# Kernel optimization log

Hardware: AMD Instinct MI355X
Metric: run time of the kernel (lower is better)

## Reference

```python
import jax, jax.numpy as jnp
import numpy as np

# SparseSphereConv (graph_level=6 -> V=40962, kernel_size=9, stride=1, select_index=None)
# Pipeline: neighbor gather -> data-dependent nonzero row selection ->
# per-vertex KxK interpolation matmul -> 1xK conv (linear over C_in,K) -> scatter back.
# With stride=1 / select_index=None the static selection is the identity, so the
# dynamic nonzero selection is equivalent to computing all rows and zeroing the
# rows whose gathered features are entirely zero (selected rows are scattered back,
# unselected rows stay 0 in sparse_reset's zero-initialized output).

BS, C_IN, C_OUT, V, K = 4, 32, 32, 40962, 9

def setup_inputs() -> dict:
    key = jax.random.key(0)
    k1, k2, k3, k4, k5 = jax.random.split(key, 5)
    x = jax.random.normal(k1, (BS, C_IN, V), dtype=jnp.float32)
    index = jax.random.randint(k2, (V, K), 0, V, dtype=jnp.int32)          # neighbor ids per vertex
    itp_mat = jax.random.uniform(k3, (V, K, K), dtype=jnp.float32)         # per-vertex interpolation
    conv_w = jax.random.normal(k4, (C_OUT, C_IN, K), dtype=jnp.float32) * 0.05  # Conv2d(C_in,C_out,(1,K)) weight
    conv_b = jax.random.normal(k5, (C_OUT,), dtype=jnp.float32) * 0.05
    return {"x": x, "index": index, "itp_mat": itp_mat, "conv_w": conv_w, "conv_b": conv_b}

def reference(x, index, itp_mat, conv_w, conv_b):
    # x: [bs, C, V] -> permute(2,0,1) -> gather neighbors -> [V, K, bs, C]
    g = jnp.transpose(x, (2, 0, 1))[index]
    g = jnp.transpose(g, (3, 2, 0, 1))                      # [C, bs, V, K]  (== reshape of [C, bs*V, K])
    # sparse_prepare: keep rows whose min or max over (C, K) is nonzero (detached in torch)
    gd = jax.lax.stop_gradient(g)
    rmin = gd.min(axis=(0, 3))                              # [bs, V]
    rmax = gd.max(axis=(0, 3))                              # [bs, V]
    mask = (rmin != 0) | (rmax != 0)                        # [bs, V]
    # Interploate: [C, S, 1, K] @ [S, K, K] per row -> batched small matmul
    interp = jnp.einsum('cbvk,vkj->cbvj', g, itp_mat)       # [C, bs, V, K]
    # Conv2d with kernel (1, K): contraction over (C_in, K) + bias
    out = jnp.einsum('cbvk,ock->bov', interp, conv_w) + conv_b[None, :, None]  # [bs, C_out, V]
    # sparse_reset: rows not selected stay zero
    return out * mask[:, None, :].astype(out.dtype)
```

## Files before the change

### kernel.cpp

```cpp
#include <hip/hip_runtime.h>
#include <hip/hip_bf16.h>

#define NV 40962
#define NK 9
#define CIN 32
#define COUT 32
#define NBS 4
#define VT 256
#define TP 260
#define NT 2561
#define PGRID 512
#define NV81 (NV * 81)
#define NV9  (NV * 9)

typedef __attribute__((ext_vector_type(8))) short bf16x8;
typedef __attribute__((ext_vector_type(4))) float f32x4;
typedef __attribute__((ext_vector_type(2))) float f32x2;

#define PKFMA_L(A, G, R) asm("v_pk_fma_f32 %0, %1, %2, %0 op_sel:[0,0,0] op_sel_hi:[0,1,1]" : "+v"(A) : "v"(G), "v"(R))
#define PKFMA_H(A, G, R) asm("v_pk_fma_f32 %0, %1, %2, %0 op_sel:[1,0,0] op_sel_hi:[1,1,1]" : "+v"(A) : "v"(G), "v"(R))
#define PKMUL_L(A, G, R) asm("v_pk_mul_f32 %0, %1, %2 op_sel:[0,0] op_sel_hi:[0,1]" : "=v"(A) : "v"(G), "v"(R))
#define PKMUL_H(A, G, R) asm("v_pk_mul_f32 %0, %1, %2 op_sel:[1,0] op_sel_hi:[1,1]" : "=v"(A) : "v"(G), "v"(R))

#define ACC(cc, j) ((j) == 8 ? acc8[cc] : (((j) & 1) ? acc2[cc][(j) >> 1].y \
                                                     : acc2[cc][(j) >> 1].x))

__device__ __forceinline__ unsigned pkbf(float a, float b) {
    union { __hip_bfloat162 h2; unsigned u; } cv;
    cv.h2 = __float22bfloat162_rn(make_float2(a, b));
    return cv.u;
}

__device__ __forceinline__ void bar_lgkm() {
    asm volatile("s_waitcnt lgkmcnt(0)\n\ts_barrier" ::: "memory");
}

__global__ void __launch_bounds__(256) transpose_x_bf16(
    const float* __restrict__ x, unsigned* __restrict__ xtw)
{
    __shared__ unsigned T[16 * TP];
    const int b  = blockIdx.x & 3;
    const int v0 = (blockIdx.x >> 2) * VT;
    const int t  = threadIdx.x;
    const int w  = t >> 6;
    const int L  = t & 63;
    const bool full = (v0 + VT <= NV);

    #pragma unroll
    for (int i = 0; i < 4; ++i) {
        const int q = w + 4 * i;
        const float* rowA = x + (size_t)(b * 32 + 2 * q) * NV;
        const float* rowB = rowA + NV;
        #pragma unroll
        for (int h = 0; h < 2; ++h) {
            const int vl = 128 * h + 2 * L;
            float2 a, c;
            if (full) {
                a = *(const float2*)(rowA + v0 + vl);
                c = *(const float2*)(rowB + v0 + vl);
            } else {
                const int v = v0 + vl;
                a.x = (v     < NV) ? rowA[v]     : 0.0f;
                a.y = (v + 1 < NV) ? rowA[v + 1] : 0.0f;
                c.x = (v     < NV) ? rowB[v]     : 0.0f;
                c.y = (v + 1 < NV) ? rowB[v + 1] : 0.0f;
            }
            uint2 d;
            d.x = pkbf(a.x, c.x);
            d.y = pkbf(a.y, c.y);
            *(uint2*)&T[q * TP + vl] = d;
        }
    }
    __syncthreads();

    #pragma unroll
    for (int i = 0; i < 4; ++i) {
        const int vl = i * 64 + w * 16 + (L >> 2);
        const int u4 = L & 3;
        const int v  = v0 + vl;
        if (v < NV) {
            uint4 d;
            d.x = T[(4 * u4 + 0) * TP + vl];
            d.y = T[(4 * u4 + 1) * TP + vl];
            d.z = T[(4 * u4 + 2) * TP + vl];
            d.w = T[(4 * u4 + 3) * TP + vl];
            *(uint4*)&xtw[(size_t)v * 64 + b * 16 + 4 * u4] = d;
        }
    }
}

__device__ __forceinline__ void load_itp(float itpv[3],
                                         const float* __restrict__ itp,
                                         int tile, int t)
{
    const size_t base = (size_t)tile * 1296;
    #pragma unroll
    for (int i = 0; i < 3; ++i) {
        const int o = i * 512 + t;
        itpv[i] = (o < 1296 && base + o < (size_t)NV81) ? itp[base + o] : 0.0f;
    }
}

__device__ __forceinline__ void stage_itp(float* __restrict__ buf,
                                          const float itpv[3], int t)
{
    #pragma unroll
    for (int i = 0; i < 3; ++i) {
        const int o = i * 512 + t;
        if (o < 1296) {
            const int vl = o / 81;
            const int r  = o - vl * 81;
            const int kk = r / 9;
            const int jj = r - kk * 9;
            buf[vl * 108 + kk * 12 + jj] = itpv[i];
        }
    }
}

__device__ __forceinline__ int load_idx(const int* __restrict__ index,
                                        int tile, int t)
{
    int r = 0;
    if (t < 144) {
        const size_t base = (size_t)tile * 144 + t;
        r = (base < (size_t)NV9) ? index[base] : 0;
    }
    return r;
}

__global__ void __launch_bounds__(512) sparse_conv_mfma(
    const unsigned short* __restrict__ xt, const int* __restrict__ index,
    const float* __restrict__ itp, const float* __restrict__ w,
    const float* __restrict__ bias, float* __restrict__ out)
{
    __shared__ unsigned Alds8[72 * 64 * 2];
    __shared__ unsigned short Wlds[36 * 32 * 8];
    __shared__ float itp_s[16 * 108];
    __shared__ int   idx_s[2][144];
    __shared__ unsigned long long nzb[8];

    const int t    = threadIdx.x;
    const int col  = t & 63;
    const int q    = t >> 6;
    const int b    = col >> 4;
    const int vloc = col & 15;
    const unsigned short* gb = xt + b * 32 + q * 4;

    int tile = blockIdx.x;

    #pragma unroll
    for (int r = 0; r < 3; ++r) {
        const int j = t + r * 512;
        if (j < 1152) {
            const int o = j & 31;
            const int c = j >> 5;
            const float4 f0 = *(const float4*)(w + o * 288 + c * 8);
            const float4 f1 = *(const float4*)(w + o * 288 + c * 8 + 4);
            uint4 d;
            d.x = pkbf(f0.x, f0.y); d.y = pkbf(f0.z, f0.w);
            d.z = pkbf(f1.x, f1.y); d.w = pkbf(f1.z, f1.w);
            *(uint4*)&Wlds[(c * 32 + o) * 8] = d;
        }
    }
    {
        const int i0 = load_idx(index, tile, t);
        const int i1 = load_idx(index, min(tile + PGRID, NT - 1), t);
        if (t < 144) { idx_s[0][t] = i0; idx_s[1][t] = i1; }
    }
    float itpv[3];
    load_itp(itpv, itp, tile, t);
    stage_itp(itp_s, itpv, t);
    __syncthreads();

    uint2 gath[NK];
    #pragma unroll
    for (int k = 0; k < NK; ++k) {
        const int nbr = idx_s[0][vloc * 9 + k];
        gath[k] = *(const uint2*)(gb + (size_t)nbr * 128);
    }
    load_itp(itpv, itp, min(tile + PGRID, NT - 1), t);
    int idxn = load_idx(index, min(tile + 2 * PGRID, NT - 1), t);
    int cur = 0;

    for (; tile < NT; tile += PGRID) {
        unsigned nzbits = 0;
        f32x2 acc2[4][4];
        float acc8[4];
        const float* ib = &itp_s[vloc * 108];

        #pragma unroll
        for (int k = 0; k < 4; ++k) {
            const uint2 gk = gath[k];
            nzbits |= (gk.x | gk.y) & 0x7FFF7FFFu;
            f32x2 gp01, gp23;
            gp01.x = __uint_as_float(gk.x << 16);
            gp01.y = __uint_as_float(gk.x & 0xFFFF0000u);
            gp23.x = __uint_as_float(gk.y << 16);
            gp23.y = __uint_as_float(gk.y & 0xFFFF0000u);
            const float* ir = ib + k * 12;
            f32x2 rp[4];
            rp[0] = *(const f32x2*)ir;       rp[1] = *(const f32x2*)(ir + 2);
            rp[2] = *(const f32x2*)(ir + 4); rp[3] = *(const f32x2*)(ir + 6);
            const float r8 = ir[8];
            if (k == 0) {
                #pragma unroll
                for (int jp = 0; jp < 4; ++jp) {
                    PKMUL_L(acc2[0][jp], gp01, rp[jp]);
                    PKMUL_H(acc2[1][jp], gp01, rp[jp]);
                    PKMUL_L(acc2[2][jp], gp23, rp[jp]);
                    PKMUL_H(acc2[3][jp], gp23, rp[jp]);
                }
                acc8[0] = gp01.x * r8; acc8[1] = gp01.y * r8;
                acc8[2] = gp23.x * r8; acc8[3] = gp23.y * r8;
            } else {
                #pragma unroll
                for (int jp = 0; jp < 4; ++jp) {
                    PKFMA_L(acc2[0][jp], gp01, rp[jp]);
                    PKFMA_H(acc2[1][jp], gp01, rp[jp]);
                    PKFMA_L(acc2[2][jp], gp23, rp[jp]);
                    PKFMA_H(acc2[3][jp], gp23, rp[jp]);
                }
                acc8[0] += gp01.x * r8; acc8[1] += gp01.y * r8;
                acc8[2] += gp23.x * r8; acc8[3] += gp23.y * r8;
            }
        }
        #pragma unroll
        for (int k = 0; k < 4; ++k) {
            const int nbr = idx_s[cur ^ 1][vloc * 9 + k];
            gath[k] = *(const uint2*)(gb + (size_t)nbr * 128);
        }
        #pragma unroll
        for (int k = 4; k < 9; ++k) {
            const uint2 gk = gath[k];
            nzbits |= (gk.x | gk.y) & 0x7FFF7FFFu;
            f32x2 gp01, gp23;
            gp01.x = __uint_as_float(gk.x << 16);
            gp01.y = __uint_as_float(gk.x & 0xFFFF0000u);
            gp23.x = __uint_as_float(gk.y << 16);
            gp23.y = __uint_as_float(gk.y & 0xFFFF0000u);
            const float* ir = ib + k * 12;
            f32x2 rp[4];
            rp[0] = *(const f32x2*)ir;       rp[1] = *(const f32x2*)(ir + 2);
            rp[2] = *(const f32x2*)(ir + 4); rp[3] = *(const f32x2*)(ir + 6);
            const float r8 = ir[8];
            #pragma unroll
            for (int jp = 0; jp < 4; ++jp) {
                PKFMA_L(acc2[0][jp], gp01, rp[jp]);
                PKFMA_H(acc2[1][jp], gp01, rp[jp]);
                PKFMA_L(acc2[2][jp], gp23, rp[jp]);
                PKFMA_H(acc2[3][jp], gp23, rp[jp]);
            }
            acc8[0] += gp01.x * r8; acc8[1] += gp01.y * r8;
            acc8[2] += gp23.x * r8; acc8[3] += gp23.y * r8;
        }
        #pragma unroll
        for (int k = 4; k < 9; ++k) {
            const int nbr = idx_s[cur ^ 1][vloc * 9 + k];
            gath[k] = *(const uint2*)(gb + (size_t)nbr * 128);
        }

        #pragma unroll
        for (int i2 = 0; i2 < 9; ++i2) {
            const int k0 = 4 * i2;
            const int h  = 9 * q + i2;
            uint2 d;
            d.x = pkbf(ACC(k0 / 9, k0 % 9),
                       ACC((k0 + 1) / 9, (k0 + 1) % 9));
            d.y = pkbf(ACC((k0 + 2) / 9, (k0 + 2) % 9),
                       ACC((k0 + 3) / 9, (k0 + 3) % 9));
            *(uint2*)&Alds8[(h * 64 + col) * 2] = d;
        }
        const unsigned long long bal = __ballot(nzbits != 0);
        if (col == 0) nzb[q] = bal;

        bar_lgkm();

        {
            const int dq = b;
            const int bb = q >> 1;
            const int oh = q & 1;
            const int colw = bb * 16 + vloc;

            f32x4 a0 = {0.f, 0.f, 0.f, 0.f};
            #pragma unroll
            for (int ks = 0; ks < 9; ++ks) {
                const int h0 = ks * 8 + dq * 2;
                const uint2 l2 = *(const uint2*)&Alds8[(h0 * 64 + colw) * 2];
                const uint2 h2 = *(const uint2*)&Alds8[((h0 + 1) * 64 + colw) * 2];
                union { uint4 u; bf16x8 v; } f;
                f.u.x = l2.x; f.u.y = l2.y; f.u.z = h2.x; f.u.w = h2.y;
                const int ch = ks * 4 + dq;
                const bf16x8 wa = *(const bf16x8*)&Wlds[(ch * 32 + oh * 16 + vloc) * 8];
                a0 = __builtin_amdgcn_mfma_f32_16x16x32_bf16(wa, f.v, a0, 0, 0, 0);
            }

            const unsigned long long nz = nzb[0] | nzb[1] | nzb[2] | nzb[3] |
                                          nzb[4] | nzb[5] | nzb[6] | nzb[7];
            const float m = ((nz >> colw) & 1ull) ? 1.0f : 0.0f;
            const int vv = tile * 16 + vloc;
            if (vv < NV) {
                float* outb = out + (size_t)bb * (COUT * NV) + vv;
                #pragma unroll
                for (int r = 0; r < 4; ++r) {
                    const int o = oh * 16 + dq * 4 + r;
                    outb[(size_t)o * NV] = (a0[r] + bias[o]) * m;
                }
            }
        }
        stage_itp(itp_s, itpv, t);
        if (t < 144) idx_s[cur][t] = idxn;
        load_itp(itpv, itp, min(tile + 2 * PGRID, NT - 1), t);
        idxn = load_idx(index, min(tile + 3 * PGRID, NT - 1), t);

        bar_lgkm();
        cur ^= 1;
    }
}

extern "C" void kernel_launch(void* const* d_in, const int* in_sizes, int n_in,
                              void* d_out, int out_size, void* d_ws, size_t ws_size,
                              hipStream_t stream)
{
    const float* x     = (const float*)d_in[0];
    const int*   index = (const int*)  d_in[1];
    const float* itp   = (const float*)d_in[2];
    const float* w     = (const float*)d_in[3];
    const float* bias  = (const float*)d_in[4];
    float*       out   = (float*)d_out;

    unsigned short* xt = (unsigned short*)d_ws;

    const int vtiles = (NV + VT - 1) / VT;
    hipLaunchKernelGGL(transpose_x_bf16, dim3(vtiles * NBS), dim3(256), 0,
                       stream, x, (unsigned*)xt);
    hipLaunchKernelGGL(sparse_conv_mfma, dim3(PGRID), dim3(512), 0,
                       stream, xt, index, itp, w, bias, out);
}
```

Measured before the change: 129.9 us.

## Move weight bf16 conversion to pre-kernel, remap waves per batch, raise grid

```diff
diff --git a/kernel.cpp b/kernel.cpp
--- a/kernel.cpp
+++ b/kernel.cpp
@@ -9,7 +9,7 @@
 #define VT 256
 #define TP 260
 #define NT 2561
-#define PGRID 512
+#define PGRID 768
 #define NV81 (NV * 81)
 #define NV9  (NV * 9)
 
@@ -89,6 +89,16 @@
     }
 }
 
+__global__ void __launch_bounds__(256) convert_w_bf16(
+    const float* __restrict__ w, unsigned short* __restrict__ wbf)
+{
+    const int i = blockIdx.x * 256 + threadIdx.x;
+    if (i < COUT * CIN * NK) {
+        unsigned u = __float_as_uint(w[i]);
+        wbf[i] = (unsigned short)((u + 0x7FFFu + ((u >> 16) & 1u)) >> 16);
+    }
+}
+
 __device__ __forceinline__ void load_itp(float itpv[3],
                                          const float* __restrict__ itp,
                                          int tile, int t)
@@ -130,38 +140,25 @@
 
 __global__ void __launch_bounds__(512) sparse_conv_mfma(
     const unsigned short* __restrict__ xt, const int* __restrict__ index,
-    const float* __restrict__ itp, const float* __restrict__ w,
+    const float* __restrict__ itp, const unsigned short* __restrict__ wbf,
     const float* __restrict__ bias, float* __restrict__ out)
 {
     __shared__ unsigned Alds8[72 * 64 * 2];
-    __shared__ unsigned short Wlds[36 * 32 * 8];
     __shared__ float itp_s[16 * 108];
     __shared__ int   idx_s[2][144];
     __shared__ unsigned long long nzb[8];
 
     const int t    = threadIdx.x;
-    const int col  = t & 63;
-    const int q    = t >> 6;
-    const int b    = col >> 4;
-    const int vloc = col & 15;
-    const unsigned short* gb = xt + b * 32 + q * 4;
+    const int wv   = t >> 6;
+    const int b    = wv >> 1;
+    const int half = wv & 1;
+    const int lane = t & 63;
+    const int vloc = lane & 15;
+    const int quad = lane >> 4;
+    const int col  = b * 16 + vloc;
+    const unsigned short* gb = xt + b * 32 + half * 16 + quad * 4;
 
     int tile = blockIdx.x;
-
-    #pragma unroll
-    for (int r = 0; r < 3; ++r) {
-        const int j = t + r * 512;
-        if (j < 1152) {
-            const int o = j & 31;
-            const int c = j >> 5;
-            const float4 f0 = *(const float4*)(w + o * 288 + c * 8);
-            const float4 f1 = *(const float4*)(w + o * 288 + c * 8 + 4);
-            uint4 d;
-            d.x = pkbf(f0.x, f0.y); d.y = pkbf(f0.z, f0.w);
-            d.z = pkbf(f1.x, f1.y); d.w = pkbf(f1.z, f1.w);
-            *(uint4*)&Wlds[(c * 32 + o) * 8] = d;
-        }
-    }
     {
         const int i0 = load_idx(index, tile, t);
         const int i1 = load_idx(index, min(tile + PGRID, NT - 1), t);
@@ -262,47 +259,44 @@
         #pragma unroll
         for (int i2 = 0; i2 < 9; ++i2) {
             const int k0 = 4 * i2;
-            const int h  = 9 * q + i2;
+            const int pl = 36 * half + 9 * quad + i2;
             uint2 d;
             d.x = pkbf(ACC(k0 / 9, k0 % 9),
                        ACC((k0 + 1) / 9, (k0 + 1) % 9));
             d.y = pkbf(ACC((k0 + 2) / 9, (k0 + 2) % 9),
                        ACC((k0 + 3) / 9, (k0 + 3) % 9));
-            *(uint2*)&Alds8[(h * 64 + col) * 2] = d;
-        }
-        const unsigned long long bal = __ballot(nzbits != 0);
-        if (col == 0) nzb[q] = bal;
+            *(uint2*)&Alds8[(pl * 64 + col) * 2] = d;
+        }
+        unsigned nzw = nzbits;
+        nzw |= __shfl_xor(nzw, 16);
+        nzw |= __shfl_xor(nzw, 32);
+        const unsigned long long bal = __ballot(nzw != 0);
+        if (lane == 0) nzb[wv] = bal;
 
         bar_lgkm();
 
         {
-            const int dq = b;
-            const int bb = q >> 1;
-            const int oh = q & 1;
-            const int colw = bb * 16 + vloc;
-
             f32x4 a0 = {0.f, 0.f, 0.f, 0.f};
             #pragma unroll
             for (int ks = 0; ks < 9; ++ks) {
-                const int h0 = ks * 8 + dq * 2;
-                const uint2 l2 = *(const uint2*)&Alds8[(h0 * 64 + colw) * 2];
-                const uint2 h2 = *(const uint2*)&Alds8[((h0 + 1) * 64 + colw) * 2];
+                const int p0 = ks * 8 + quad * 2;
+                const uint2 l2 = *(const uint2*)&Alds8[(p0 * 64 + col) * 2];
+                const uint2 h2 = *(const uint2*)&Alds8[((p0 + 1) * 64 + col) * 2];
                 union { uint4 u; bf16x8 v; } f;
                 f.u.x = l2.x; f.u.y = l2.y; f.u.z = h2.x; f.u.w = h2.y;
-                const int ch = ks * 4 + dq;
-                const bf16x8 wa = *(const bf16x8*)&Wlds[(ch * 32 + oh * 16 + vloc) * 8];
+                const int ko = ks * 32 + quad * 8;
+                const bf16x8 wa = *(const bf16x8*)(wbf + (half * 16 + vloc) * 288 + ko);
                 a0 = __builtin_amdgcn_mfma_f32_16x16x32_bf16(wa, f.v, a0, 0, 0, 0);
             }
 
-            const unsigned long long nz = nzb[0] | nzb[1] | nzb[2] | nzb[3] |
-                                          nzb[4] | nzb[5] | nzb[6] | nzb[7];
-            const float m = ((nz >> colw) & 1ull) ? 1.0f : 0.0f;
+            const unsigned long long nz = nzb[2 * b] | nzb[2 * b + 1];
+            const float m = ((nz >> vloc) & 1ull) ? 1.0f : 0.0f;
             const int vv = tile * 16 + vloc;
             if (vv < NV) {
-                float* outb = out + (size_t)bb * (COUT * NV) + vv;
+                float* outb = out + (size_t)b * (COUT * NV) + vv;
                 #pragma unroll
                 for (int r = 0; r < 4; ++r) {
-                    const int o = oh * 16 + dq * 4 + r;
+                    const int o = half * 16 + quad * 4 + r;
                     outb[(size_t)o * NV] = (a0[r] + bias[o]) * m;
                 }
             }
@@ -328,11 +322,14 @@
     const float* bias  = (const float*)d_in[4];
     float*       out   = (float*)d_out;
 
-    unsigned short* xt = (unsigned short*)d_ws;
-
+    unsigned short* xt  = (unsigned short*)d_ws;
+    unsigned short* wbf = (unsigned short*)((char*)d_ws + (size_t)NV * 256);
+
+    hipLaunchKernelGGL(convert_w_bf16, dim3((COUT * CIN * NK + 255) / 256),
+                       dim3(256), 0, stream, w, wbf);
     const int vtiles = (NV + VT - 1) / VT;
     hipLaunchKernelGGL(transpose_x_bf16, dim3(vtiles * NBS), dim3(256), 0,
                        stream, x, (unsigned*)xt);
     hipLaunchKernelGGL(sparse_conv_mfma, dim3(PGRID), dim3(512), 0,
-                       stream, xt, index, itp, w, bias, out);
-}
+                       stream, xt, index, itp, wbf, bias, out);
+}
```

Measured after the change: 143.9 us. 10.8% more time.
